# Kernel optimization log

Hardware: AMD Instinct MI355X
Metric: run time of the kernel (lower is better)

The kernel has to match this reference:

```python
import jax, jax.numpy as jnp
import numpy as np

D_MODEL = 1024
N_HEADS = 16
HEAD_DIM = D_MODEL // N_HEADS
WINDOW = 128
ROPE_BASE = 10000.0


def _rope_cos_sin(T, dim, dtype):
    inv_freq = 1.0 / (ROPE_BASE ** (jnp.arange(0, dim, 2, dtype=jnp.float32) / dim))
    freqs = jnp.arange(T, dtype=jnp.float32)[:, None] * inv_freq[None, :]  # [T, dim/2]
    emb = jnp.concatenate([freqs, freqs], axis=-1)  # [T, dim]
    return jnp.cos(emb).astype(dtype), jnp.sin(emb).astype(dtype)


def _rotate_half(x):
    h = x.shape[-1] // 2
    return jnp.concatenate([-x[..., h:], x[..., :h]], axis=-1)


def _apply_rotary(x, cos, sin):
    # x: [B, T, H, Dh]; cos/sin: [T, Dh]
    c = cos[None, :, None, :]
    s = sin[None, :, None, :]
    return x * c + _rotate_half(x) * s


def setup_inputs() -> dict:
    key = jax.random.key(0)
    ks = jax.random.split(key, 6)
    B, T = 2, 2048
    query = jax.random.normal(ks[0], (B, T, D_MODEL), dtype=jnp.float32)
    scale = 1.0 / np.sqrt(D_MODEL)
    Wq = jax.random.normal(ks[1], (D_MODEL, D_MODEL), dtype=jnp.float32) * scale
    Wk = jax.random.normal(ks[2], (D_MODEL, D_MODEL), dtype=jnp.float32) * scale
    Wv = jax.random.normal(ks[3], (D_MODEL, D_MODEL), dtype=jnp.float32) * scale
    Wo = jax.random.normal(ks[4], (D_MODEL, D_MODEL), dtype=jnp.float32) * scale
    bo = jax.random.normal(ks[5], (D_MODEL,), dtype=jnp.float32) * 0.01
    return {"query": query, "Wq": Wq, "Wk": Wk, "Wv": Wv, "Wo": Wo, "bo": bo}


def reference(query, Wq, Wk, Wv, Wo, bo):
    # Sliding-window causal self-attention with rotary embeddings (eval mode, no dropout).
    B, T, D = query.shape
    H, Dh = N_HEADS, HEAD_DIM
    sm_scale = Dh ** -0.5

    # Projections (torch nn.Linear: y = x @ W.T)
    q = (query @ Wq.T).reshape(B, T, H, Dh)
    k = (query @ Wk.T).reshape(B, T, H, Dh)
    v = (query @ Wv.T).reshape(B, T, H, Dh)

    cos, sin = _rope_cos_sin(T, Dh, query.dtype)
    q = _apply_rotary(q, cos, sin)
    k = _apply_rotary(k, cos, sin)

    # [B, H, T, Dh]
    q = q.transpose(0, 2, 1, 3)
    k = k.transpose(0, 2, 1, 3)
    v = v.transpose(0, 2, 1, 3)

    scores = jnp.einsum('bhqd,bhkd->bhqk', q, k) * sm_scale

    # Causal sliding-window mask: masked if j > i or j < i - (WINDOW - 1)
    i = jnp.arange(T)[:, None]
    j = jnp.arange(T)[None, :]
    mask = (j > i) | (j < i - (WINDOW - 1))  # [T, T], True = masked
    scores = jnp.where(mask[None, None], jnp.float32(-jnp.inf), scores)

    attn = jax.nn.softmax(scores, axis=-1)
    out = jnp.einsum('bhqk,bhkd->bhqd', attn, v)  # [B, H, T, Dh]
    out = out.transpose(0, 2, 1, 3).reshape(B, T, D)
    return out @ Wo.T + bo
```

## Files before the change

### kernel.cpp

```cpp
#include <hip/hip_runtime.h>

#define BATCH 2
#define SEQ   2048
#define DMODEL 1024
#define NHEADS 16
#define HDIM   64
#define WINDOW 128
#define ROWS  (BATCH * SEQ)

typedef __bf16 bf16x8 __attribute__((ext_vector_type(8)));
typedef __bf16 bf16x4 __attribute__((ext_vector_type(4)));
typedef float  f32x4  __attribute__((ext_vector_type(4)));

__global__ __launch_bounds__(256) void convert_bf16(
    const float* __restrict__ X,
    const float* __restrict__ Wq, const float* __restrict__ Wk,
    const float* __restrict__ Wv, const float* __restrict__ Wo,
    __bf16* __restrict__ Xbf, __bf16* __restrict__ Wbf)
{
    const int XN = ROWS * DMODEL / 4;
    const int WN = DMODEL * DMODEL / 4;
    int idx = blockIdx.x * blockDim.x + threadIdx.x;
    if (idx >= XN + 4 * WN) return;

    const float* src;
    __bf16* dst;
    if (idx < XN) {
        src = X + (size_t)idx * 4;
        dst = Xbf + (size_t)idx * 4;
    } else {
        int rel = idx - XN;
        int w = rel / WN;
        int off = rel - w * WN;
        const float* Wp = (w == 0) ? Wq : (w == 1) ? Wk : (w == 2) ? Wv : Wo;
        src = Wp + (size_t)off * 4;
        dst = Wbf + (size_t)rel * 4;
    }
    float4 v = *(const float4*)src;
    bf16x4 o;
    o[0] = (__bf16)v.x; o[1] = (__bf16)v.y; o[2] = (__bf16)v.z; o[3] = (__bf16)v.w;
    *(bf16x4*)dst = o;
}

__global__ __launch_bounds__(256) void rope_table(float* __restrict__ ct,
                                                  float* __restrict__ st)
{
    int idx = blockIdx.x * blockDim.x + threadIdx.x;
    if (idx >= SEQ * 32) return;
    int t = idx >> 5, d = idx & 31;
    float ang = (float)t * expf(-(float)d * 0.28782313662425572f);
    float s, c;
    sincosf(ang, &s, &c);
    ct[idx] = c; st[idx] = s;
}

#define LDK 40

__device__ __forceinline__ void gemm_mfma_body(
    const __bf16* __restrict__ A, const __bf16* __restrict__ B,
    void* __restrict__ Cout, const float* __restrict__ bias,
    const float* __restrict__ ct, const float* __restrict__ st,
    int mode, int N, int K, int m0, int n0)
{
    __shared__ __bf16 As[128 * LDK];
    __shared__ __bf16 Bs[128 * LDK];

    const int tid  = threadIdx.x;
    const int lane = tid & 63;
    const int wv   = tid >> 6;
    const int wrow = (wv >> 1) * 64;
    const int wcol = (wv & 1) * 64;

    const int srow  = tid >> 2;
    const int skoff = (tid & 3) * 8;

    const int frow = lane & 15;
    const int fk   = (lane >> 4) * 8;

    f32x4 acc[4][4];
#pragma unroll
    for (int i = 0; i < 4; ++i)
#pragma unroll
        for (int j = 0; j < 4; ++j) {
            acc[i][j][0] = 0.f; acc[i][j][1] = 0.f;
            acc[i][j][2] = 0.f; acc[i][j][3] = 0.f;
        }

    for (int k0 = 0; k0 < K; k0 += 32) {
        bf16x8 av0 = *(const bf16x8*)(A + (size_t)(m0 + srow) * K + k0 + skoff);
        bf16x8 av1 = *(const bf16x8*)(A + (size_t)(m0 + 64 + srow) * K + k0 + skoff);
        bf16x8 bv0 = *(const bf16x8*)(B + (size_t)(n0 + srow) * K + k0 + skoff);
        bf16x8 bv1 = *(const bf16x8*)(B + (size_t)(n0 + 64 + srow) * K + k0 + skoff);
        __syncthreads();
        *(bf16x8*)(As + srow * LDK + skoff) = av0;
        *(bf16x8*)(As + (64 + srow) * LDK + skoff) = av1;
        *(bf16x8*)(Bs + srow * LDK + skoff) = bv0;
        *(bf16x8*)(Bs + (64 + srow) * LDK + skoff) = bv1;
        __syncthreads();

        bf16x8 afr[4], bfr[4];
#pragma unroll
        for (int i = 0; i < 4; ++i)
            afr[i] = *(const bf16x8*)(As + (wrow + i * 16 + frow) * LDK + fk);
#pragma unroll
        for (int j = 0; j < 4; ++j)
            bfr[j] = *(const bf16x8*)(Bs + (wcol + j * 16 + frow) * LDK + fk);
#pragma unroll
        for (int i = 0; i < 4; ++i)
#pragma unroll
            for (int j = 0; j < 4; ++j)
                acc[i][j] = __builtin_amdgcn_mfma_f32_16x16x32_bf16(
                    afr[i], bfr[j], acc[i][j], 0, 0, 0);
    }

#pragma unroll
    for (int i = 0; i < 4; ++i) {
#pragma unroll
        for (int r = 0; r < 4; ++r) {
            int row = m0 + wrow + i * 16 + (lane >> 4) * 4 + r;
            if (mode <= 1) {
                int t = row & (SEQ - 1);
#pragma unroll
                for (int j = 0; j < 2; ++j) {
                    int dd = j * 16 + (lane & 15);
                    float c = ct[t * 32 + dd];
                    float s = st[t * 32 + dd];
                    float v0 = acc[i][j][r], v1 = acc[i][j + 2][r];
                    float n0v = v0 * c - v1 * s;
                    float n1v = v1 * c + v0 * s;
                    if (mode == 0) { n0v *= 0.125f; n1v *= 0.125f; }
                    acc[i][j][r] = n0v; acc[i][j + 2][r] = n1v;
                }
            }
#pragma unroll
            for (int j = 0; j < 4; ++j) {
                int col = n0 + wcol + j * 16 + (lane & 15);
                float v = acc[i][j][r];
                if (mode == 3)
                    ((float*)Cout)[(size_t)row * N + col] = v + bias[col];
                else
                    ((__bf16*)Cout)[(size_t)row * N + col] = (__bf16)v;
            }
        }
    }
}

__global__ __launch_bounds__(256) void gemm_qkv_bf(
    const __bf16* __restrict__ X, const __bf16* __restrict__ Wbf,
    __bf16* __restrict__ Qb, __bf16* __restrict__ Kb, __bf16* __restrict__ Vb,
    const float* __restrict__ ct, const float* __restrict__ st)
{
    const int z = blockIdx.z;
    const __bf16* W = Wbf + (size_t)z * (DMODEL * DMODEL);
    __bf16* C = (z == 0) ? Qb : (z == 1) ? Kb : Vb;
    gemm_mfma_body(X, W, C, nullptr, ct, st, z, DMODEL, DMODEL,
                   blockIdx.y * 128, blockIdx.x * 128);
}

__global__ __launch_bounds__(256) void gemm_out_bf(
    const __bf16* __restrict__ Abf, const __bf16* __restrict__ Wo,
    const float* __restrict__ bias, float* __restrict__ out)
{
    gemm_mfma_body(Abf, Wo, out, bias, nullptr, nullptr, 3, DMODEL, DMODEL,
                   blockIdx.y * 128, blockIdx.x * 128);
}

#define QTILE 64
#define KPAD  72
#define VPAD  216
#define PPAD  168

__global__ __launch_bounds__(256) void attn_mfma(
    const __bf16* __restrict__ Qb, const __bf16* __restrict__ Kb,
    const __bf16* __restrict__ Vb, __bf16* __restrict__ Abf)
{
    __shared__ __bf16 KsPs[192 * KPAD];
    __shared__ __bf16 Vt[64 * VPAD];

    const int tid  = threadIdx.x;
    const int lane = tid & 63;
    const int wv   = tid >> 6;
    const int q0   = blockIdx.x * QTILE;
    const int h    = blockIdx.y;
    const int b    = blockIdx.z;
    const int jbase = q0 - 128;
    const size_t hoff = (size_t)h * HDIM;
    const int nloc  = lane & 15;
    const int mbase = (lane >> 4) * 4;
    const int fk    = (lane >> 4) * 8;

    const __bf16* Kg = Kb + (size_t)(b * SEQ) * DMODEL + hoff;
    const __bf16* Vg = Vb + (size_t)(b * SEQ) * DMODEL + hoff;

#pragma unroll
    for (int it = 0; it < 6; ++it) {
        int idx = tid + it * 256;
        int jt = idx >> 3;
        int dq = (idx & 7) * 8;
        int jg = jbase + jt;
        int jc = jg < 0 ? 0 : jg;
        bf16x8 kv = *(const bf16x8*)(Kg + (size_t)jc * DMODEL + dq);
        bf16x8 vv = *(const bf16x8*)(Vg + (size_t)jc * DMODEL + dq);
        *(bf16x8*)(KsPs + jt * KPAD + dq) = kv;
#pragma unroll
        for (int e = 0; e < 8; ++e) Vt[(dq + e) * VPAD + jt] = vv[e];
    }
#pragma unroll
    for (int it = 0; it < 4; ++it) {
        int idx = tid + it * 256;
        int d = idx >> 4, c = idx & 15;
        Vt[d * VPAD + 192 + c] = (__bf16)0.0f;
    }
    __syncthreads();

    const __bf16* Qg = Qb + (size_t)(b * SEQ + q0 + 16 * wv + nloc) * DMODEL + hoff + fk;
    bf16x8 qfr0 = *(const bf16x8*)(Qg);
    bf16x8 qfr1 = *(const bf16x8*)(Qg + 32);

    f32x4 s[9];
#pragma unroll
    for (int c = 0; c < 9; ++c) {
        const __bf16* kp = KsPs + (size_t)(16 * (wv + c) + nloc) * KPAD + fk;
        bf16x8 k0 = *(const bf16x8*)kp;
        bf16x8 k1 = *(const bf16x8*)(kp + 32);
        f32x4 z; z[0] = 0.f; z[1] = 0.f; z[2] = 0.f; z[3] = 0.f;
        z = __builtin_amdgcn_mfma_f32_16x16x32_bf16(qfr0, k0, z, 0, 0, 0);
        z = __builtin_amdgcn_mfma_f32_16x16x32_bf16(qfr1, k1, z, 0, 0, 0);
        s[c] = z;
    }
    __syncthreads();

    float inv_row[4];
#pragma unroll
    for (int r = 0; r < 4; ++r) {
        int rl = 16 * wv + mbase + r;
        float mx = -INFINITY;
#pragma unroll
        for (int c = 0; c < 9; ++c) {
            int jt = 16 * (wv + c) + nloc;
            bool valid = (jt >= rl + 1) && (jt <= rl + 128) && (jbase + jt >= 0);
            float sv = valid ? s[c][r] : -INFINITY;
            s[c][r] = sv;
            mx = fmaxf(mx, sv);
        }
#pragma unroll
        for (int off = 8; off; off >>= 1) mx = fmaxf(mx, __shfl_xor(mx, off));
        float sum = 0.f;
#pragma unroll
        for (int c = 0; c < 9; ++c) {
            float p = __expf(s[c][r] - mx);
            s[c][r] = p;
            sum += p;
        }
#pragma unroll
        for (int off = 8; off; off >>= 1) sum += __shfl_xor(sum, off);
        inv_row[r] = 1.0f / sum;
    }

    __bf16* myP = KsPs + (size_t)wv * 16 * PPAD;
#pragma unroll
    for (int c = 0; c < 9; ++c)
#pragma unroll
        for (int r = 0; r < 4; ++r)
            myP[(mbase + r) * PPAD + 16 * c + nloc] = (__bf16)(s[c][r] * inv_row[r]);
#pragma unroll
    for (int r = 0; r < 4; ++r)
        myP[(mbase + r) * PPAD + 144 + nloc] = (__bf16)0.0f;

    asm volatile("" ::: "memory");
    __builtin_amdgcn_s_waitcnt(0);

    f32x4 o[4];
#pragma unroll
    for (int j = 0; j < 4; ++j) { o[j][0] = 0.f; o[j][1] = 0.f; o[j][2] = 0.f; o[j][3] = 0.f; }
#pragma unroll
    for (int stp = 0; stp < 5; ++stp) {
        bf16x8 pf = *(const bf16x8*)(myP + nloc * PPAD + 32 * stp + fk);
#pragma unroll
        for (int j = 0; j < 4; ++j) {
            bf16x8 vf = *(const bf16x8*)(Vt + (size_t)(16 * j + nloc) * VPAD
                                         + 16 * wv + 32 * stp + fk);
            o[j] = __builtin_amdgcn_mfma_f32_16x16x32_bf16(pf, vf, o[j], 0, 0, 0);
        }
    }

    __bf16* Og = Abf + (size_t)(b * SEQ + q0 + 16 * wv) * DMODEL + hoff;
#pragma unroll
    for (int j = 0; j < 4; ++j)
#pragma unroll
        for (int r = 0; r < 4; ++r)
            Og[(size_t)(mbase + r) * DMODEL + 16 * j + nloc] = (__bf16)o[j][r];
}

extern "C" void kernel_launch(void* const* d_in, const int* in_sizes, int n_in,
                              void* d_out, int out_size, void* d_ws, size_t ws_size,
                              hipStream_t stream)
{
    const float* X  = (const float*)d_in[0];
    const float* Wq = (const float*)d_in[1];
    const float* Wk = (const float*)d_in[2];
    const float* Wv = (const float*)d_in[3];
    const float* Wo = (const float*)d_in[4];
    const float* bo = (const float*)d_in[5];
    float* out = (float*)d_out;

    const size_t MB = 1ull << 20;
    __bf16* Xbf = (__bf16*)d_ws;
    __bf16* Wbf = (__bf16*)((char*)d_ws + 8 * MB);
    __bf16* Qb  = (__bf16*)((char*)d_ws + 16 * MB);
    __bf16* Kb  = (__bf16*)((char*)d_ws + 24 * MB);
    __bf16* Vb  = (__bf16*)((char*)d_ws + 32 * MB);
    float*  ctab = (float*)((char*)d_ws + 40 * MB);
    float*  stab = (float*)((char*)d_ws + 41 * MB);
    __bf16* Abf = Xbf;

    {
        int groups = (ROWS * DMODEL + 4 * DMODEL * DMODEL) / 4;
        convert_bf16<<<(groups + 255) / 256, 256, 0, stream>>>(
            X, Wq, Wk, Wv, Wo, Xbf, Wbf);
    }
    {
        rope_table<<<(SEQ * 32 + 255) / 256, 256, 0, stream>>>(ctab, stab);
    }
    {
        dim3 grid(DMODEL / 128, ROWS / 128, 3);
        gemm_qkv_bf<<<grid, 256, 0, stream>>>(Xbf, Wbf, Qb, Kb, Vb, ctab, stab);
    }
    {
        dim3 grid(SEQ / QTILE, NHEADS, BATCH);
        attn_mfma<<<grid, 256, 0, stream>>>(Qb, Kb, Vb, Abf);
    }
    {
        dim3 grid(DMODEL / 128, ROWS / 128, 1);
        gemm_out_bf<<<grid, 256, 0, stream>>>(Abf, Wbf + 3ull * DMODEL * DMODEL, bo, out);
    }
}
```

Measured before the change: 188.5 us.

## Use direct global-to-LDS loads with XOR swizzle in GEMM; fuse rope table into convert

Result: faster. 184.7 us (-2.0%).

```diff
diff --git a/kernel.cpp b/kernel.cpp
--- a/kernel.cpp
+++ b/kernel.cpp
@@ -12,49 +12,51 @@
 typedef __bf16 bf16x4 __attribute__((ext_vector_type(4)));
 typedef float  f32x4  __attribute__((ext_vector_type(4)));
 
+__device__ __forceinline__ void async_load16(const __bf16* g, __bf16* l) {
+    __builtin_amdgcn_global_load_lds(
+        (const __attribute__((address_space(1))) unsigned int*)g,
+        (__attribute__((address_space(3))) unsigned int*)l, 16, 0, 0);
+}
+
 __global__ __launch_bounds__(256) void convert_bf16(
     const float* __restrict__ X,
     const float* __restrict__ Wq, const float* __restrict__ Wk,
     const float* __restrict__ Wv, const float* __restrict__ Wo,
-    __bf16* __restrict__ Xbf, __bf16* __restrict__ Wbf)
+    __bf16* __restrict__ Xbf, __bf16* __restrict__ Wbf,
+    float* __restrict__ ct, float* __restrict__ st)
 {
     const int XN = ROWS * DMODEL / 4;
     const int WN = DMODEL * DMODEL / 4;
+    const int TOT = XN + 4 * WN;
     int idx = blockIdx.x * blockDim.x + threadIdx.x;
-    if (idx >= XN + 4 * WN) return;
-
-    const float* src;
-    __bf16* dst;
-    if (idx < XN) {
-        src = X + (size_t)idx * 4;
-        dst = Xbf + (size_t)idx * 4;
-    } else {
-        int rel = idx - XN;
-        int w = rel / WN;
-        int off = rel - w * WN;
-        const float* Wp = (w == 0) ? Wq : (w == 1) ? Wk : (w == 2) ? Wv : Wo;
-        src = Wp + (size_t)off * 4;
-        dst = Wbf + (size_t)rel * 4;
-    }
-    float4 v = *(const float4*)src;
-    bf16x4 o;
-    o[0] = (__bf16)v.x; o[1] = (__bf16)v.y; o[2] = (__bf16)v.z; o[3] = (__bf16)v.w;
-    *(bf16x4*)dst = o;
-}
-
-__global__ __launch_bounds__(256) void rope_table(float* __restrict__ ct,
-                                                  float* __restrict__ st)
-{
-    int idx = blockIdx.x * blockDim.x + threadIdx.x;
-    if (idx >= SEQ * 32) return;
-    int t = idx >> 5, d = idx & 31;
-    float ang = (float)t * expf(-(float)d * 0.28782313662425572f);
-    float s, c;
-    sincosf(ang, &s, &c);
-    ct[idx] = c; st[idx] = s;
-}
-
-#define LDK 40
+
+    if (idx < TOT) {
+        const float* src;
+        __bf16* dst;
+        if (idx < XN) {
+            src = X + (size_t)idx * 4;
+            dst = Xbf + (size_t)idx * 4;
+        } else {
+            int rel = idx - XN;
+            int w = rel / WN;
+            int off = rel - w * WN;
+            const float* Wp = (w == 0) ? Wq : (w == 1) ? Wk : (w == 2) ? Wv : Wo;
+            src = Wp + (size_t)off * 4;
+            dst = Wbf + (size_t)rel * 4;
+        }
+        float4 v = *(const float4*)src;
+        bf16x4 o;
+        o[0] = (__bf16)v.x; o[1] = (__bf16)v.y; o[2] = (__bf16)v.z; o[3] = (__bf16)v.w;
+        *(bf16x4*)dst = o;
+    } else if (idx < TOT + SEQ * 32) {
+        int k = idx - TOT;
+        int t = k >> 5, d = k & 31;
+        float ang = (float)t * expf(-(float)d * 0.28782313662425572f);
+        float s, c;
+        sincosf(ang, &s, &c);
+        ct[k] = c; st[k] = s;
+    }
+}
 
 __device__ __forceinline__ void gemm_mfma_body(
     const __bf16* __restrict__ A, const __bf16* __restrict__ B,
@@ -62,8 +64,8 @@
     const float* __restrict__ ct, const float* __restrict__ st,
     int mode, int N, int K, int m0, int n0)
 {
-    __shared__ __bf16 As[128 * LDK];
-    __shared__ __bf16 Bs[128 * LDK];
+    __shared__ __bf16 As[128 * 32];
+    __shared__ __bf16 Bs[128 * 32];
 
     const int tid  = threadIdx.x;
     const int lane = tid & 63;
@@ -71,11 +73,21 @@
     const int wrow = (wv >> 1) * 64;
     const int wcol = (wv & 1) * 64;
 
-    const int srow  = tid >> 2;
-    const int skoff = (tid & 3) * 8;
+    const int srow = lane >> 2;
+    const int schk = (lane & 3) ^ ((lane >> 3) & 3);
+    const int rbase = 32 * wv;
+
+    const __bf16* gA0 = A + (size_t)(m0 + rbase + srow) * K + 8 * schk;
+    const __bf16* gA1 = gA0 + (size_t)16 * K;
+    const __bf16* gB0 = B + (size_t)(n0 + rbase + srow) * K + 8 * schk;
+    const __bf16* gB1 = gB0 + (size_t)16 * K;
+    __bf16* lA0 = As + rbase * 32;
+    __bf16* lA1 = lA0 + 16 * 32;
+    __bf16* lB0 = Bs + rbase * 32;
+    __bf16* lB1 = lB0 + 16 * 32;
 
     const int frow = lane & 15;
-    const int fk   = (lane >> 4) * 8;
+    const int fsw  = 8 * ((lane >> 4) ^ ((frow >> 1) & 3));
 
     f32x4 acc[4][4];
 #pragma unroll
@@ -87,24 +99,20 @@
         }
 
     for (int k0 = 0; k0 < K; k0 += 32) {
-        bf16x8 av0 = *(const bf16x8*)(A + (size_t)(m0 + srow) * K + k0 + skoff);
-        bf16x8 av1 = *(const bf16x8*)(A + (size_t)(m0 + 64 + srow) * K + k0 + skoff);
-        bf16x8 bv0 = *(const bf16x8*)(B + (size_t)(n0 + srow) * K + k0 + skoff);
-        bf16x8 bv1 = *(const bf16x8*)(B + (size_t)(n0 + 64 + srow) * K + k0 + skoff);
         __syncthreads();
-        *(bf16x8*)(As + srow * LDK + skoff) = av0;
-        *(bf16x8*)(As + (64 + srow) * LDK + skoff) = av1;
-        *(bf16x8*)(Bs + srow * LDK + skoff) = bv0;
-        *(bf16x8*)(Bs + (64 + srow) * LDK + skoff) = bv1;
+        async_load16(gA0 + k0, lA0);
+        async_load16(gA1 + k0, lA1);
+        async_load16(gB0 + k0, lB0);
+        async_load16(gB1 + k0, lB1);
         __syncthreads();
 
         bf16x8 afr[4], bfr[4];
 #pragma unroll
         for (int i = 0; i < 4; ++i)
-            afr[i] = *(const bf16x8*)(As + (wrow + i * 16 + frow) * LDK + fk);
+            afr[i] = *(const bf16x8*)(As + (wrow + 16 * i + frow) * 32 + fsw);
 #pragma unroll
         for (int j = 0; j < 4; ++j)
-            bfr[j] = *(const bf16x8*)(Bs + (wcol + j * 16 + frow) * LDK + fk);
+            bfr[j] = *(const bf16x8*)(Bs + (wcol + 16 * j + frow) * 32 + fsw);
 #pragma unroll
         for (int i = 0; i < 4; ++i)
 #pragma unroll
@@ -315,12 +323,9 @@
     __bf16* Abf = Xbf;
 
     {
-        int groups = (ROWS * DMODEL + 4 * DMODEL * DMODEL) / 4;
-        convert_bf16<<<(groups + 255) / 256, 256, 0, stream>>>(
-            X, Wq, Wk, Wv, Wo, Xbf, Wbf);
-    }
-    {
-        rope_table<<<(SEQ * 32 + 255) / 256, 256, 0, stream>>>(ctab, stab);
+        int total = (ROWS * DMODEL + 4 * DMODEL * DMODEL) / 4 + SEQ * 32;
+        convert_bf16<<<(total + 255) / 256, 256, 0, stream>>>(
+            X, Wq, Wk, Wv, Wo, Xbf, Wbf, ctab, stab);
     }
     {
         dim3 grid(DMODEL / 128, ROWS / 128, 3);
```
